# Performance work log

Measured on AMD Instinct MI355X. Metric: run time of the kernel, lower is better.

Reference implementation:

```python
import jax, jax.numpy as jnp
import numpy as np
import math

NUM_HEADS = 16
HEAD_DIM = 64
EMBED = 1024
NUM_BUCKETS = 32
MAX_DISTANCE = 128


def _relative_position_bucket(relative_position, num_buckets=NUM_BUCKETS, max_distance=MAX_DISTANCE):
    # bidirectional T5 bucketing
    nb = num_buckets // 2
    relative_buckets = (relative_position > 0).astype(jnp.int32) * nb
    rp = jnp.abs(relative_position)
    max_exact = nb // 2
    is_small = rp < max_exact
    rp_safe = jnp.maximum(rp, 1)  # avoid log(0); masked by is_small anyway
    rp_large = max_exact + (
        jnp.log(rp_safe.astype(jnp.float32) / max_exact)
        / math.log(max_distance / max_exact)
        * (nb - max_exact)
    ).astype(jnp.int32)
    rp_large = jnp.minimum(rp_large, nb - 1)
    return relative_buckets + jnp.where(is_small, rp, rp_large)


def compute_bias(rel_emb, q_len, k_len):
    ctx = jnp.arange(q_len)[:, None]
    mem = jnp.arange(k_len)[None, :]
    buckets = _relative_position_bucket(mem - ctx)  # [q,k]
    values = rel_emb[buckets]                       # [q,k,H]
    return jnp.transpose(values, (2, 0, 1))[None]   # [1,H,q,k]


def setup_inputs() -> dict:
    key = jax.random.key(0)
    ks = jax.random.split(key, 6)
    std = 0.02
    B, S = 2, 2048
    inner = NUM_HEADS * HEAD_DIM
    return {
        "input_ids": jax.random.normal(ks[0], (B, S, EMBED), dtype=jnp.float32),
        "Wq": jax.random.normal(ks[1], (EMBED, inner), dtype=jnp.float32) * std,
        "Wk": jax.random.normal(ks[2], (EMBED, inner), dtype=jnp.float32) * std,
        "Wv": jax.random.normal(ks[3], (EMBED, inner), dtype=jnp.float32) * std,
        "Wo": jax.random.normal(ks[4], (inner, EMBED), dtype=jnp.float32) * std,
        "rel_emb": jax.random.normal(ks[5], (NUM_BUCKETS, NUM_HEADS), dtype=jnp.float32) * std,
    }


def reference(input_ids, Wq, Wk, Wv, Wo, rel_emb):
    B, S, _ = input_ids.shape
    H, D = NUM_HEADS, HEAD_DIM
    q = (input_ids @ Wq).reshape(B, S, H, D).transpose(0, 2, 1, 3)  # [B,H,S,D]
    k = (input_ids @ Wk).reshape(B, S, H, D).transpose(0, 2, 1, 3)
    v = (input_ids @ Wv).reshape(B, S, H, D).transpose(0, 2, 1, 3)
    scores = jnp.einsum("bhqd,bhkd->bhqk", q, k)  # no 1/sqrt(d) scaling (T5 style)
    position_bias = compute_bias(rel_emb, S, S)   # [1,H,S,S]
    scores = scores + position_bias
    attn = jax.nn.softmax(scores, axis=-1)
    out = jnp.einsum("bhqk,bhkd->bhqd", attn, v)
    out = out.transpose(0, 2, 1, 3).reshape(B, S, H * D)
    out = out @ Wo
    return out, position_bias
```

## Files before the change

kernel.cpp:

```cpp
#include <hip/hip_runtime.h>
#include <stdint.h>

#define S_LEN 2048
#define NH 16
#define EMB 1024

typedef __attribute__((ext_vector_type(8))) short bf16x8;
typedef __attribute__((ext_vector_type(4))) float floatx4;
typedef const __attribute__((address_space(1))) unsigned int* gas_u32p;
typedef __attribute__((address_space(3))) unsigned int* las_u32p;

static __device__ __forceinline__ void gld_lds16(const void* g, void* l) {
  __builtin_amdgcn_global_load_lds((gas_u32p)g, (las_u32p)l, 16, 0, 0);
}

static __device__ __forceinline__ unsigned short f2bf(float f) {
  unsigned int u = __float_as_uint(f);
  unsigned int r = (u + 0x7FFFu + ((u >> 16) & 1u)) >> 16;
  return (unsigned short)r;
}
static __device__ __forceinline__ unsigned short f2bf_fast(float f) {
  return (unsigned short)((__float_as_uint(f) + 0x8000u) >> 16);
}

__global__ void cast_x_kernel(const float* __restrict__ x, unsigned short* __restrict__ out, int n4) {
  int i = blockIdx.x * blockDim.x + threadIdx.x;
  if (i >= n4) return;
  float4 v = ((const float4*)x)[i];
  ushort4 o;
  o.x = f2bf(v.x); o.y = f2bf(v.y); o.z = f2bf(v.z); o.w = f2bf(v.w);
  ((ushort4*)out)[i] = o;
}

__global__ void transpose_cast3(const float* __restrict__ W0, const float* __restrict__ W1,
                                const float* __restrict__ W2, unsigned short* __restrict__ out) {
  __shared__ float tile[32][33];
  const float* in = (blockIdx.z == 0) ? W0 : ((blockIdx.z == 1) ? W1 : W2);
  unsigned short* o = out + (size_t)blockIdx.z * 1048576;
  int x = blockIdx.x * 32 + threadIdx.x;
  int y0 = blockIdx.y * 32 + threadIdx.y;
#pragma unroll
  for (int j = 0; j < 4; j++)
    tile[threadIdx.y + 8 * j][threadIdx.x] = in[(y0 + 8 * j) * EMB + x];
  __syncthreads();
  int x2 = blockIdx.y * 32 + threadIdx.x;
  int y2 = blockIdx.x * 32 + threadIdx.y;
#pragma unroll
  for (int j = 0; j < 4; j++)
    o[(y2 + 8 * j) * EMB + x2] = f2bf(tile[threadIdx.x][threadIdx.y + 8 * j]);
}

__global__ void build_lut_kernel(const float* __restrict__ rel_emb, float* __restrict__ lut) {
  int idx = blockIdx.x * blockDim.x + threadIdx.x;
  if (idx >= 4096) return;
  int delta = idx - 2048;
  int bucket = (delta > 0) ? 16 : 0;
  int rp = (delta < 0) ? -delta : delta;
  int bl;
  if (rp < 8) bl = rp;
  else bl = 8 + (rp >= 12) + (rp >= 16) + (rp >= 23) + (rp >= 32) + (rp >= 46) + (rp >= 64) + (rp >= 91);
  bucket += bl;
#pragma unroll
  for (int h = 0; h < NH; h++)
    lut[h * 4096 + idx] = rel_emb[bucket * NH + h];
}

__global__ void bias_out_kernel(const float* __restrict__ lut, float* __restrict__ dst) {
  int i = blockIdx.x * blockDim.x + threadIdx.x;
  int h = i >> 20;
  int rem = i & 1048575;
  int q = rem >> 9;
  int k4 = (rem & 511) << 2;
  const float* lr = lut + h * 4096 + (k4 - q + 2048);
  float4 v = make_float4(__ldg(lr), __ldg(lr + 1), __ldg(lr + 2), __ldg(lr + 3));
  ((float4*)dst)[i] = v;
}

__global__ __launch_bounds__(256) void gemm_qk(const unsigned short* __restrict__ A,
                                               const unsigned short* __restrict__ BT,
                                               unsigned short* __restrict__ oQ,
                                               unsigned short* __restrict__ oK) {
  __shared__ __align__(16) unsigned short As[128 * 64];
  __shared__ __align__(16) unsigned short Bs[128 * 64];
  const int tid = threadIdx.x;
  const int wave = tid >> 6, lane = tid & 63;
  const int quad = lane >> 4, lm = lane & 15;
  const int wm = wave & 1, wn = wave >> 1;
  const int mBase = blockIdx.y * 128, nBase = blockIdx.x * 128;
  const int gg = (lane & 7) ^ (lane >> 3);
  const int srow = lane >> 3;
  floatx4 acc[4][4];
#pragma unroll
  for (int i = 0; i < 4; i++)
#pragma unroll
    for (int j = 0; j < 4; j++) acc[i][j] = (floatx4){0.f, 0.f, 0.f, 0.f};

  for (int kt = 0; kt < 16; kt++) {
    int k0 = kt * 64;
    __syncthreads();
#pragma unroll
    for (int c = 0; c < 4; c++) {
      int chunk = wave * 4 + c;
      int row = chunk * 8 + srow;
      gld_lds16(&A[(size_t)(mBase + row) * 1024 + k0 + gg * 8], &As[chunk * 512]);
      gld_lds16(&BT[(size_t)(nBase + row) * 1024 + k0 + gg * 8], &Bs[chunk * 512]);
    }
    __syncthreads();
#pragma unroll
    for (int hh = 0; hh < 2; hh++) {
      bf16x8 af[4], bfr[4];
#pragma unroll
      for (int i = 0; i < 4; i++)
        af[i] = *(const bf16x8*)&As[(wm * 64 + i * 16 + lm) * 64 + (((hh << 2) + quad) ^ (lm & 7)) * 8];
#pragma unroll
      for (int j = 0; j < 4; j++)
        bfr[j] = *(const bf16x8*)&Bs[(wn * 64 + j * 16 + lm) * 64 + (((hh << 2) + quad) ^ (lm & 7)) * 8];
#pragma unroll
      for (int i = 0; i < 4; i++)
#pragma unroll
        for (int j = 0; j < 4; j++)
          acc[i][j] = __builtin_amdgcn_mfma_f32_16x16x32_bf16(af[i], bfr[j], acc[i][j], 0, 0, 0);
    }
  }
  const int which = nBase >> 10;
#pragma unroll
  for (int i = 0; i < 4; i++)
#pragma unroll
    for (int j = 0; j < 4; j++)
#pragma unroll
      for (int r = 0; r < 4; r++) {
        int row = mBase + wm * 64 + i * 16 + quad * 4 + r;
        int col = nBase + wn * 64 + j * 16 + lm;
        int b = row >> 11, s = row & 2047;
        int cw = col & 1023;
        int h = cw >> 6, d = cw & 63;
        unsigned short v = f2bf(acc[i][j][r]);
        if (which == 0) oQ[(((size_t)(b * NH + h) * S_LEN + s) * 64) + d] = v;
        else            oK[(((size_t)(b * NH + h) * S_LEN + s) * 64) + d] = v;
      }
}

__global__ __launch_bounds__(256) void gemm_v(const unsigned short* __restrict__ A,
                                              const unsigned short* __restrict__ BT,
                                              unsigned short* __restrict__ oV) {
  __shared__ __align__(16) unsigned short As[128 * 64];
  __shared__ __align__(16) unsigned short Bs[128 * 64];
  const int tid = threadIdx.x;
  const int wave = tid >> 6, lane = tid & 63;
  const int quad = lane >> 4, lm = lane & 15;
  const int wm = wave & 1, wn = wave >> 1;
  const int mBase = blockIdx.y * 128, nBase = blockIdx.x * 128;
  const int gg = (lane & 7) ^ (lane >> 3);
  const int srow = lane >> 3;
  floatx4 acc[4][4];
#pragma unroll
  for (int i = 0; i < 4; i++)
#pragma unroll
    for (int j = 0; j < 4; j++) acc[i][j] = (floatx4){0.f, 0.f, 0.f, 0.f};

  for (int kt = 0; kt < 16; kt++) {
    int k0 = kt * 64;
    __syncthreads();
#pragma unroll
    for (int c = 0; c < 4; c++) {
      int chunk = wave * 4 + c;
      int row = chunk * 8 + srow;
      gld_lds16(&A[(size_t)(mBase + row) * 1024 + k0 + gg * 8], &As[chunk * 512]);
      gld_lds16(&BT[(size_t)(nBase + row) * 1024 + k0 + gg * 8], &Bs[chunk * 512]);
    }
    __syncthreads();
#pragma unroll
    for (int hh = 0; hh < 2; hh++) {
      bf16x8 af[4], bfr[4];
#pragma unroll
      for (int i = 0; i < 4; i++)
        af[i] = *(const bf16x8*)&As[(wm * 64 + i * 16 + lm) * 64 + (((hh << 2) + quad) ^ (lm & 7)) * 8];
#pragma unroll
      for (int j = 0; j < 4; j++)
        bfr[j] = *(const bf16x8*)&Bs[(wn * 64 + j * 16 + lm) * 64 + (((hh << 2) + quad) ^ (lm & 7)) * 8];
#pragma unroll
      for (int i = 0; i < 4; i++)
#pragma unroll
        for (int j = 0; j < 4; j++)
          acc[i][j] = __builtin_amdgcn_mfma_f32_16x16x32_bf16(bfr[j], af[i], acc[i][j], 0, 0, 0);
    }
  }
#pragma unroll
  for (int i = 0; i < 4; i++)
#pragma unroll
    for (int j = 0; j < 4; j++)
#pragma unroll
      for (int r = 0; r < 4; r++) {
        int n = nBase + wn * 64 + j * 16 + quad * 4 + r;
        int m = mBase + wm * 64 + i * 16 + lm;
        int h = n >> 6, d = n & 63;
        int b = m >> 11, s = m & 2047;
        oV[(((size_t)(b * NH + h) * 64 + d) * S_LEN) + s] = f2bf(acc[i][j][r]);
      }
}

__global__ __launch_bounds__(256) void gemm_out(const unsigned short* __restrict__ A,
                                                const unsigned short* __restrict__ BT,
                                                float* __restrict__ oF) {
  __shared__ __align__(16) unsigned short As[128 * 64];
  __shared__ __align__(16) unsigned short Bs[128 * 64];
  const int tid = threadIdx.x;
  const int wave = tid >> 6, lane = tid & 63;
  const int quad = lane >> 4, lm = lane & 15;
  const int wm = wave & 1, wn = wave >> 1;
  const int mBase = blockIdx.y * 128, nBase = blockIdx.x * 128;
  const int gg = (lane & 7) ^ (lane >> 3);
  const int srow = lane >> 3;
  floatx4 acc[4][4];
#pragma unroll
  for (int i = 0; i < 4; i++)
#pragma unroll
    for (int j = 0; j < 4; j++) acc[i][j] = (floatx4){0.f, 0.f, 0.f, 0.f};

  for (int kt = 0; kt < 16; kt++) {
    int k0 = kt * 64;
    __syncthreads();
#pragma unroll
    for (int c = 0; c < 4; c++) {
      int chunk = wave * 4 + c;
      int row = chunk * 8 + srow;
      gld_lds16(&A[(size_t)(mBase + row) * 1024 + k0 + gg * 8], &As[chunk * 512]);
      gld_lds16(&BT[(size_t)(nBase + row) * 1024 + k0 + gg * 8], &Bs[chunk * 512]);
    }
    __syncthreads();
#pragma unroll
    for (int hh = 0; hh < 2; hh++) {
      bf16x8 af[4], bfr[4];
#pragma unroll
      for (int i = 0; i < 4; i++)
        af[i] = *(const bf16x8*)&As[(wm * 64 + i * 16 + lm) * 64 + (((hh << 2) + quad) ^ (lm & 7)) * 8];
#pragma unroll
      for (int j = 0; j < 4; j++)
        bfr[j] = *(const bf16x8*)&Bs[(wn * 64 + j * 16 + lm) * 64 + (((hh << 2) + quad) ^ (lm & 7)) * 8];
#pragma unroll
      for (int i = 0; i < 4; i++)
#pragma unroll
        for (int j = 0; j < 4; j++)
          acc[i][j] = __builtin_amdgcn_mfma_f32_16x16x32_bf16(af[i], bfr[j], acc[i][j], 0, 0, 0);
    }
  }
#pragma unroll
  for (int i = 0; i < 4; i++)
#pragma unroll
    for (int j = 0; j < 4; j++)
#pragma unroll
      for (int r = 0; r < 4; r++) {
        int row = mBase + wm * 64 + i * 16 + quad * 4 + r;
        int col = nBase + wn * 64 + j * 16 + lm;
        oF[(size_t)row * 1024 + col] = acc[i][j][r];
      }
}

__global__ __launch_bounds__(512, 4) void attn_kernel(const unsigned short* __restrict__ Qb,
                                                      const unsigned short* __restrict__ Kb,
                                                      const unsigned short* __restrict__ Vtb,
                                                      const float* __restrict__ lut,
                                                      unsigned short* __restrict__ Ob) {
  __shared__ __align__(16) unsigned short Kl[2][64 * 64];
  __shared__ __align__(16) unsigned short Vl[2][64 * 64];
  __shared__ __align__(16) unsigned short Pl[8][16 * 72];
  __shared__ float lutS[512];
  const int tid = threadIdx.x;
  const int wave = tid >> 6, lane = tid & 63;
  const int quad = lane >> 4, lm = lane & 15;
  const int ws = wave & 3, half = wave >> 2;
  const int ii = blockIdx.x;
  const int bh = (ii & 7) * 4 + ((ii >> 3) & 3);
  const int qTile = (ii >> 5) * 128;
  const int b = bh >> 4, h = bh & 15;
  const unsigned short* Qp = Qb + (size_t)bh * S_LEN * 64;
  const unsigned short* Kp = Kb + (size_t)bh * S_LEN * 64;
  const unsigned short* Vp = Vtb + (size_t)bh * 64 * S_LEN;
  const float* lrow = lut + h * 4096;
  const float cneg = lrow[0], cpos = lrow[4095];
  const int gg = (lane & 7) ^ (lane >> 3);
  const int srow = lane >> 3;
  const int qw = qTile + ws * 32;

  if (tid < 512) lutS[tid] = lrow[2048 - 256 + tid];

  bf16x8 aq[2][2];
#pragma unroll
  for (int g = 0; g < 2; g++)
#pragma unroll
    for (int hh = 0; hh < 2; hh++)
      aq[g][hh] = *(const bf16x8*)&Qp[(qw + g * 16 + lm) * 64 + hh * 32 + quad * 8];

  floatx4 accO[2][4];
#pragma unroll
  for (int g = 0; g < 2; g++)
#pragma unroll
    for (int d = 0; d < 4; d++) accO[g][d] = (floatx4){0.f, 0.f, 0.f, 0.f};
  float lp[2] = {0.f, 0.f};

  unsigned short* Pw = Pl[wave];

  for (int ktl = 0; ktl < 16; ktl++) {
    const int kBase = (half << 10) + ktl * 64;
    __syncthreads();
#pragma unroll
    for (int c = 0; c < 2; c++) {
      int chunk = ws * 2 + c;
      int row = chunk * 8 + srow;
      gld_lds16(&Kp[(size_t)(kBase + row) * 64 + gg * 8], &Kl[half][chunk * 512]);
      gld_lds16(&Vp[(size_t)row * S_LEN + kBase + gg * 8], &Vl[half][chunk * 512]);
    }
    __syncthreads();

    const bool farTile = (kBase + 154 <= qTile) || (kBase >= qTile + 218);
    const float cfar = (kBase < qTile) ? cneg : cpos;

    floatx4 s4[2][4];
#pragma unroll
    for (int nt = 0; nt < 4; nt++) {
      int rbase = (nt * 16 + lm) * 64;
      bf16x8 kf0 = *(const bf16x8*)&Kl[half][rbase + ((quad ^ (lm & 7)) << 3)];
      bf16x8 kf1 = *(const bf16x8*)&Kl[half][rbase + (((4 + quad) ^ (lm & 7)) << 3)];
#pragma unroll
      for (int g = 0; g < 2; g++) {
        floatx4 z = (floatx4){0.f, 0.f, 0.f, 0.f};
        z = __builtin_amdgcn_mfma_f32_16x16x32_bf16(kf0, aq[g][0], z, 0, 0, 0);
        z = __builtin_amdgcn_mfma_f32_16x16x32_bf16(kf1, aq[g][1], z, 0, 0, 0);
        s4[g][nt] = z;
      }
    }

    bf16x8 pa[2][2];
#pragma unroll
    for (int g = 0; g < 2; g++) {
      const int b0 = kBase + quad * 4 - (qw + g * 16 + lm) + 256;
      float psum = 0.f;
#pragma unroll
      for (int nt = 0; nt < 4; nt++) {
        union { unsigned short u[4]; uint2 v; } pk;
#pragma unroll
        for (int r = 0; r < 4; r++) {
          float sv;
          if (farTile) sv = s4[g][nt][r] + cfar;
          else         sv = s4[g][nt][r] + lutS[b0 + nt * 16 + r];
          float p = __expf(sv);
          psum += p;
          pk.u[r] = f2bf_fast(p);
        }
        *(uint2*)&Pw[lm * 72 + nt * 16 + quad * 4] = pk.v;
      }
      lp[g] += psum;
      pa[g][0] = *(const bf16x8*)&Pw[lm * 72 + quad * 8];
      pa[g][1] = *(const bf16x8*)&Pw[lm * 72 + 32 + quad * 8];
    }

#pragma unroll
    for (int d = 0; d < 4; d++) {
      int rbase = (d * 16 + lm) * 64;
      bf16x8 vf0 = *(const bf16x8*)&Vl[half][rbase + ((quad ^ (lm & 7)) << 3)];
      bf16x8 vf1 = *(const bf16x8*)&Vl[half][rbase + (((4 + quad) ^ (lm & 7)) << 3)];
      accO[0][d] = __builtin_amdgcn_mfma_f32_16x16x32_bf16(pa[0][0], vf0, accO[0][d], 0, 0, 0);
      accO[0][d] = __builtin_amdgcn_mfma_f32_16x16x32_bf16(pa[0][1], vf1, accO[0][d], 0, 0, 0);
      accO[1][d] = __builtin_amdgcn_mfma_f32_16x16x32_bf16(pa[1][0], vf0, accO[1][d], 0, 0, 0);
      accO[1][d] = __builtin_amdgcn_mfma_f32_16x16x32_bf16(pa[1][1], vf1, accO[1][d], 0, 0, 0);
    }
  }

#pragma unroll
  for (int g = 0; g < 2; g++) {
    lp[g] += __shfl_xor(lp[g], 16, 64);
    lp[g] += __shfl_xor(lp[g], 32, 64);
  }

  __syncthreads();
  float* Ox = (ws < 2) ? ((float*)&Kl[0][0]) + ws * 2048 : ((float*)&Vl[0][0]) + (ws - 2) * 2048;
  float* lpf = (float*)&Pl[0][0];
  if (half == 1) {
#pragma unroll
    for (int g = 0; g < 2; g++) {
#pragma unroll
      for (int d = 0; d < 4; d++)
#pragma unroll
        for (int r = 0; r < 4; r++)
          Ox[(g * 16 + quad * 4 + r) * 64 + d * 16 + lm] = accO[g][d][r];
      if (quad == 0) lpf[ws * 32 + g * 16 + lm] = lp[g];
    }
  }
  __syncthreads();
  if (half == 0) {
    float ltot[2];
#pragma unroll
    for (int g = 0; g < 2; g++) ltot[g] = lp[g] + lpf[ws * 32 + g * 16 + lm];
#pragma unroll
    for (int g = 0; g < 2; g++) {
      float linv[4];
#pragma unroll
      for (int r = 0; r < 4; r++) linv[r] = 1.f / __shfl(ltot[g], quad * 4 + r, 64);
#pragma unroll
      for (int d = 0; d < 4; d++)
#pragma unroll
        for (int r = 0; r < 4; r++) {
          float val = accO[g][d][r] + Ox[(g * 16 + quad * 4 + r) * 64 + d * 16 + lm];
          int q = qw + g * 16 + quad * 4 + r;
          int col = h * 64 + d * 16 + lm;
          Ob[((size_t)(b * S_LEN + q)) * 1024 + col] = f2bf_fast(val * linv[r]);
        }
    }
  }
}

extern "C" void kernel_launch(void* const* d_in, const int* in_sizes, int n_in,
                              void* d_out, int out_size, void* d_ws, size_t ws_size,
                              hipStream_t stream) {
  const float* X   = (const float*)d_in[0];
  const float* Wq  = (const float*)d_in[1];
  const float* Wk  = (const float*)d_in[2];
  const float* Wv  = (const float*)d_in[3];
  const float* Wo  = (const float*)d_in[4];
  const float* rel = (const float*)d_in[5];
  float* out = (float*)d_out;
  float* bias_out = out + 4194304;

  char* ws = (char*)d_ws;
  unsigned short* Xb    = (unsigned short*)(ws);
  unsigned short* WqkvT = (unsigned short*)(ws + (size_t)(8u  << 20));
  unsigned short* WoT   = (unsigned short*)(ws + (size_t)(14u << 20));
  unsigned short* Qb    = (unsigned short*)(ws + (size_t)(16u << 20));
  unsigned short* Kb    = (unsigned short*)(ws + (size_t)(24u << 20));
  unsigned short* Vtb   = (unsigned short*)(ws + (size_t)(32u << 20));
  unsigned short* Ob    = (unsigned short*)(ws + (size_t)(40u << 20));
  float* lut            = (float*)(ws + (size_t)(48u << 20));

  cast_x_kernel<<<4096, 256, 0, stream>>>(X, Xb, 1048576);
  dim3 tb(32, 8);
  transpose_cast3<<<dim3(32, 32, 3), tb, 0, stream>>>(Wq, Wk, Wv, WqkvT);
  transpose_cast3<<<dim3(32, 32, 1), tb, 0, stream>>>(Wo, Wo, Wo, WoT);
  build_lut_kernel<<<16, 256, 0, stream>>>(rel, lut);
  bias_out_kernel<<<65536, 256, 0, stream>>>(lut, bias_out);

  gemm_qk<<<dim3(16, 32), 256, 0, stream>>>(Xb, WqkvT, Qb, Kb);
  gemm_v<<<dim3(8, 32), 256, 0, stream>>>(Xb, WqkvT + 2 * 1048576, Vtb);
  attn_kernel<<<512, 512, 0, stream>>>(Qb, Kb, Vtb, lut, Ob);
  gemm_out<<<dim3(8, 32), 256, 0, stream>>>(Ob, WoT, out);
}
```

Before: 452.4 us.

## Merge prep kernels, fuse QKV projection, switch softmax to exp2

Combines the input cast, the four weight transposes and the LUT build into one launch, and merges the Q/K and V projection GEMMs into a single 24-column-block launch whose V epilogue writes packed 4-element stores. Q and the bias LUT are pre-scaled by log2(e) so the attention softmax can use the hardware exp2 instruction instead of __expf. This cuts launch overhead and per-element exp cost. Folding the scale into bf16 Q adds a small extra rounding error.

```diff
diff --git a/kernel.cpp b/kernel.cpp
--- a/kernel.cpp
+++ b/kernel.cpp
@@ -4,6 +4,7 @@
 #define S_LEN 2048
 #define NH 16
 #define EMB 1024
+#define L2E 1.44269504f
 
 typedef __attribute__((ext_vector_type(8))) short bf16x8;
 typedef __attribute__((ext_vector_type(4))) float floatx4;
@@ -23,46 +24,51 @@
   return (unsigned short)((__float_as_uint(f) + 0x8000u) >> 16);
 }
 
-__global__ void cast_x_kernel(const float* __restrict__ x, unsigned short* __restrict__ out, int n4) {
-  int i = blockIdx.x * blockDim.x + threadIdx.x;
-  if (i >= n4) return;
-  float4 v = ((const float4*)x)[i];
-  ushort4 o;
-  o.x = f2bf(v.x); o.y = f2bf(v.y); o.z = f2bf(v.z); o.w = f2bf(v.w);
-  ((ushort4*)out)[i] = o;
-}
-
-__global__ void transpose_cast3(const float* __restrict__ W0, const float* __restrict__ W1,
-                                const float* __restrict__ W2, unsigned short* __restrict__ out) {
+__global__ __launch_bounds__(256) void prep_kernel(const float* __restrict__ X,
+                                                   const float* __restrict__ Wq,
+                                                   const float* __restrict__ Wk,
+                                                   const float* __restrict__ Wv,
+                                                   const float* __restrict__ Wo,
+                                                   const float* __restrict__ rel,
+                                                   unsigned short* __restrict__ Xb,
+                                                   unsigned short* __restrict__ WT,
+                                                   float* __restrict__ lut) {
   __shared__ float tile[32][33];
-  const float* in = (blockIdx.z == 0) ? W0 : ((blockIdx.z == 1) ? W1 : W2);
-  unsigned short* o = out + (size_t)blockIdx.z * 1048576;
-  int x = blockIdx.x * 32 + threadIdx.x;
-  int y0 = blockIdx.y * 32 + threadIdx.y;
-#pragma unroll
-  for (int j = 0; j < 4; j++)
-    tile[threadIdx.y + 8 * j][threadIdx.x] = in[(y0 + 8 * j) * EMB + x];
-  __syncthreads();
-  int x2 = blockIdx.y * 32 + threadIdx.x;
-  int y2 = blockIdx.x * 32 + threadIdx.y;
-#pragma unroll
-  for (int j = 0; j < 4; j++)
-    o[(y2 + 8 * j) * EMB + x2] = f2bf(tile[threadIdx.x][threadIdx.y + 8 * j]);
-}
-
-__global__ void build_lut_kernel(const float* __restrict__ rel_emb, float* __restrict__ lut) {
-  int idx = blockIdx.x * blockDim.x + threadIdx.x;
-  if (idx >= 4096) return;
-  int delta = idx - 2048;
-  int bucket = (delta > 0) ? 16 : 0;
-  int rp = (delta < 0) ? -delta : delta;
-  int bl;
-  if (rp < 8) bl = rp;
-  else bl = 8 + (rp >= 12) + (rp >= 16) + (rp >= 23) + (rp >= 32) + (rp >= 46) + (rp >= 64) + (rp >= 91);
-  bucket += bl;
-#pragma unroll
-  for (int h = 0; h < NH; h++)
-    lut[h * 4096 + idx] = rel_emb[bucket * NH + h];
+  const int bid = blockIdx.x, tid = threadIdx.x;
+  if (bid < 4096) {
+    int i = bid * 256 + tid;
+    float4 v = ((const float4*)X)[i];
+    ushort4 o;
+    o.x = f2bf(v.x); o.y = f2bf(v.y); o.z = f2bf(v.z); o.w = f2bf(v.w);
+    ((ushort4*)Xb)[i] = o;
+  } else if (bid < 8192) {
+    int w = (bid - 4096) >> 10, t = (bid - 4096) & 1023;
+    const float* in = (w == 0) ? Wq : (w == 1) ? Wk : (w == 2) ? Wv : Wo;
+    unsigned short* o = WT + (size_t)w * 1048576;
+    int bx = t & 31, by = t >> 5;
+    int tx = tid & 31, ty = tid >> 5;
+    int x = bx * 32 + tx, y0 = by * 32 + ty;
+#pragma unroll
+    for (int j = 0; j < 4; j++)
+      tile[ty + 8 * j][tx] = in[(y0 + 8 * j) * EMB + x];
+    __syncthreads();
+    int x2 = by * 32 + tx, y2 = bx * 32 + ty;
+#pragma unroll
+    for (int j = 0; j < 4; j++)
+      o[(y2 + 8 * j) * EMB + x2] = f2bf(tile[tx][ty + 8 * j]);
+  } else {
+    int idx = (bid - 8192) * 256 + tid;
+    int delta = idx - 2048;
+    int bucket = (delta > 0) ? 16 : 0;
+    int rp = (delta < 0) ? -delta : delta;
+    int bl;
+    if (rp < 8) bl = rp;
+    else bl = 8 + (rp >= 12) + (rp >= 16) + (rp >= 23) + (rp >= 32) + (rp >= 46) + (rp >= 64) + (rp >= 91);
+    bucket += bl;
+#pragma unroll
+    for (int h = 0; h < NH; h++)
+      lut[h * 4096 + idx] = rel[bucket * NH + h];
+  }
 }
 
 __global__ void bias_out_kernel(const float* __restrict__ lut, float* __restrict__ dst) {
@@ -76,10 +82,11 @@
   ((float4*)dst)[i] = v;
 }
 
-__global__ __launch_bounds__(256) void gemm_qk(const unsigned short* __restrict__ A,
-                                               const unsigned short* __restrict__ BT,
-                                               unsigned short* __restrict__ oQ,
-                                               unsigned short* __restrict__ oK) {
+__global__ __launch_bounds__(256) void gemm_qkv(const unsigned short* __restrict__ A,
+                                                const unsigned short* __restrict__ BT,
+                                                unsigned short* __restrict__ oQ,
+                                                unsigned short* __restrict__ oK,
+                                                unsigned short* __restrict__ oV) {
   __shared__ __align__(16) unsigned short As[128 * 64];
   __shared__ __align__(16) unsigned short Bs[128 * 64];
   const int tid = threadIdx.x;
@@ -123,80 +130,39 @@
     }
   }
   const int which = nBase >> 10;
-#pragma unroll
-  for (int i = 0; i < 4; i++)
-#pragma unroll
-    for (int j = 0; j < 4; j++)
-#pragma unroll
-      for (int r = 0; r < 4; r++) {
-        int row = mBase + wm * 64 + i * 16 + quad * 4 + r;
-        int col = nBase + wn * 64 + j * 16 + lm;
-        int b = row >> 11, s = row & 2047;
-        int cw = col & 1023;
-        int h = cw >> 6, d = cw & 63;
-        unsigned short v = f2bf(acc[i][j][r]);
-        if (which == 0) oQ[(((size_t)(b * NH + h) * S_LEN + s) * 64) + d] = v;
-        else            oK[(((size_t)(b * NH + h) * S_LEN + s) * 64) + d] = v;
+  if (which == 2) {
+#pragma unroll
+    for (int i = 0; i < 4; i++)
+#pragma unroll
+      for (int j = 0; j < 4; j++) {
+        int hd = (nBase - 2048) + wn * 64 + j * 16 + lm;
+        int h = hd >> 6, d = hd & 63;
+        int m = mBase + wm * 64 + i * 16 + quad * 4;
+        int b = m >> 11, s = m & 2047;
+        union { unsigned short u[4]; uint2 v; } pk;
+#pragma unroll
+        for (int r = 0; r < 4; r++) pk.u[r] = f2bf(acc[i][j][r]);
+        *(uint2*)&oV[(((size_t)(b * NH + h) * 64 + d) * S_LEN) + s] = pk.v;
       }
-}
-
-__global__ __launch_bounds__(256) void gemm_v(const unsigned short* __restrict__ A,
-                                              const unsigned short* __restrict__ BT,
-                                              unsigned short* __restrict__ oV) {
-  __shared__ __align__(16) unsigned short As[128 * 64];
-  __shared__ __align__(16) unsigned short Bs[128 * 64];
-  const int tid = threadIdx.x;
-  const int wave = tid >> 6, lane = tid & 63;
-  const int quad = lane >> 4, lm = lane & 15;
-  const int wm = wave & 1, wn = wave >> 1;
-  const int mBase = blockIdx.y * 128, nBase = blockIdx.x * 128;
-  const int gg = (lane & 7) ^ (lane >> 3);
-  const int srow = lane >> 3;
-  floatx4 acc[4][4];
-#pragma unroll
-  for (int i = 0; i < 4; i++)
-#pragma unroll
-    for (int j = 0; j < 4; j++) acc[i][j] = (floatx4){0.f, 0.f, 0.f, 0.f};
-
-  for (int kt = 0; kt < 16; kt++) {
-    int k0 = kt * 64;
-    __syncthreads();
-#pragma unroll
-    for (int c = 0; c < 4; c++) {
-      int chunk = wave * 4 + c;
-      int row = chunk * 8 + srow;
-      gld_lds16(&A[(size_t)(mBase + row) * 1024 + k0 + gg * 8], &As[chunk * 512]);
-      gld_lds16(&BT[(size_t)(nBase + row) * 1024 + k0 + gg * 8], &Bs[chunk * 512]);
-    }
-    __syncthreads();
-#pragma unroll
-    for (int hh = 0; hh < 2; hh++) {
-      bf16x8 af[4], bfr[4];
-#pragma unroll
-      for (int i = 0; i < 4; i++)
-        af[i] = *(const bf16x8*)&As[(wm * 64 + i * 16 + lm) * 64 + (((hh << 2) + quad) ^ (lm & 7)) * 8];
+  } else {
+#pragma unroll
+    for (int i = 0; i < 4; i++)
 #pragma unroll
       for (int j = 0; j < 4; j++)
-        bfr[j] = *(const bf16x8*)&Bs[(wn * 64 + j * 16 + lm) * 64 + (((hh << 2) + quad) ^ (lm & 7)) * 8];
-#pragma unroll
-      for (int i = 0; i < 4; i++)
-#pragma unroll
-        for (int j = 0; j < 4; j++)
-          acc[i][j] = __builtin_amdgcn_mfma_f32_16x16x32_bf16(bfr[j], af[i], acc[i][j], 0, 0, 0);
-    }
-  }
-#pragma unroll
-  for (int i = 0; i < 4; i++)
-#pragma unroll
-    for (int j = 0; j < 4; j++)
-#pragma unroll
-      for (int r = 0; r < 4; r++) {
-        int n = nBase + wn * 64 + j * 16 + quad * 4 + r;
-        int m = mBase + wm * 64 + i * 16 + lm;
-        int h = n >> 6, d = n & 63;
-        int b = m >> 11, s = m & 2047;
-        oV[(((size_t)(b * NH + h) * 64 + d) * S_LEN) + s] = f2bf(acc[i][j][r]);
-      }
+#pragma unroll
+        for (int r = 0; r < 4; r++) {
+          int row = mBase + wm * 64 + i * 16 + quad * 4 + r;
+          int col = nBase + wn * 64 + j * 16 + lm;
+          int b = row >> 11, s = row & 2047;
+          int cw = col & 1023;
+          int h = cw >> 6, d = cw & 63;
+          float v = acc[i][j][r];
+          if (which == 0) v *= L2E;
+          unsigned short sv = f2bf(v);
+          if (which == 0) oQ[(((size_t)(b * NH + h) * S_LEN + s) * 64) + d] = sv;
+          else            oK[(((size_t)(b * NH + h) * S_LEN + s) * 64) + d] = sv;
+        }
+  }
 }
 
 __global__ __launch_bounds__(256) void gemm_out(const unsigned short* __restrict__ A,
@@ -277,12 +243,12 @@
   const unsigned short* Kp = Kb + (size_t)bh * S_LEN * 64;
   const unsigned short* Vp = Vtb + (size_t)bh * 64 * S_LEN;
   const float* lrow = lut + h * 4096;
-  const float cneg = lrow[0], cpos = lrow[4095];
+  const float cneg = lrow[0] * L2E, cpos = lrow[4095] * L2E;
   const int gg = (lane & 7) ^ (lane >> 3);
   const int srow = lane >> 3;
   const int qw = qTile + ws * 32;
 
-  if (tid < 512) lutS[tid] = lrow[2048 - 256 + tid];
+  lutS[tid & 511] = lrow[2048 - 256 + (tid & 511)] * L2E;
 
   bf16x8 aq[2][2];
 #pragma unroll
@@ -343,7 +309,7 @@
           float sv;
           if (farTile) sv = s4[g][nt][r] + cfar;
           else         sv = s4[g][nt][r] + lutS[b0 + nt * 16 + r];
-          float p = __expf(sv);
+          float p = __builtin_amdgcn_exp2f(sv);
           psum += p;
           pk.u[r] = f2bf_fast(p);
         }
@@ -422,24 +388,17 @@
   float* bias_out = out + 4194304;
 
   char* ws = (char*)d_ws;
-  unsigned short* Xb    = (unsigned short*)(ws);
-  unsigned short* WqkvT = (unsigned short*)(ws + (size_t)(8u  << 20));
-  unsigned short* WoT   = (unsigned short*)(ws + (size_t)(14u << 20));
-  unsigned short* Qb    = (unsigned short*)(ws + (size_t)(16u << 20));
-  unsigned short* Kb    = (unsigned short*)(ws + (size_t)(24u << 20));
-  unsigned short* Vtb   = (unsigned short*)(ws + (size_t)(32u << 20));
-  unsigned short* Ob    = (unsigned short*)(ws + (size_t)(40u << 20));
-  float* lut            = (float*)(ws + (size_t)(48u << 20));
-
-  cast_x_kernel<<<4096, 256, 0, stream>>>(X, Xb, 1048576);
-  dim3 tb(32, 8);
-  transpose_cast3<<<dim3(32, 32, 3), tb, 0, stream>>>(Wq, Wk, Wv, WqkvT);
-  transpose_cast3<<<dim3(32, 32, 1), tb, 0, stream>>>(Wo, Wo, Wo, WoT);
-  build_lut_kernel<<<16, 256, 0, stream>>>(rel, lut);
+  unsigned short* Xb  = (unsigned short*)(ws);
+  unsigned short* WT  = (unsigned short*)(ws + (size_t)(8u << 20));
+  unsigned short* Qb  = (unsigned short*)(ws + (size_t)(16u << 20));
+  unsigned short* Kb  = (unsigned short*)(ws + (size_t)(24u << 20));
+  unsigned short* Vtb = (unsigned short*)(ws + (size_t)(32u << 20));
+  unsigned short* Ob  = (unsigned short*)(ws + (size_t)(40u << 20));
+  float* lut          = (float*)(ws + (size_t)(48u << 20));
+
+  prep_kernel<<<8208, 256, 0, stream>>>(X, Wq, Wk, Wv, Wo, rel, Xb, WT, lut);
   bias_out_kernel<<<65536, 256, 0, stream>>>(lut, bias_out);
-
-  gemm_qk<<<dim3(16, 32), 256, 0, stream>>>(Xb, WqkvT, Qb, Kb);
-  gemm_v<<<dim3(8, 32), 256, 0, stream>>>(Xb, WqkvT + 2 * 1048576, Vtb);
+  gemm_qkv<<<dim3(24, 32), 256, 0, stream>>>(Xb, WT, Qb, Kb, Vtb);
   attn_kernel<<<512, 512, 0, stream>>>(Qb, Kb, Vtb, lut, Ob);
-  gemm_out<<<dim3(8, 32), 256, 0, stream>>>(Ob, WoT, out);
-}
+  gemm_out<<<dim3(8, 32), 256, 0, stream>>>(Ob, WT + 3 * 1048576, out);
+}
```

Measured after the change: 444.2 us. No clear change (-1.8%).
